# Kernel optimization log

Measured on AMD Instinct MI355X. Metric: run time of the kernel, lower is better.

The kernel has to match this reference:

```python
import jax, jax.numpy as jnp
import numpy as np

NEG_SLOPE = 0.2


def _segment_softmax(logits, seg, num_segments):
    m = jax.ops.segment_max(logits, seg, num_segments=num_segments)
    m = jnp.where(jnp.isfinite(m), m, 0.0)
    e = jnp.exp(logits - m[seg])
    s = jax.ops.segment_sum(e, seg, num_segments=num_segments)
    return e / (s[seg] + 1e-16)


def _gat_conv(x, src, dst, W, a_src, a_dst, b, num_nodes):
    # PyG GATConv, heads=1, concat=True, add_self_loops already applied to src/dst.
    h = x @ W                                  # [N, F_out]
    alpha_src = h @ a_src                      # [N]
    alpha_dst = h @ a_dst                      # [N]
    logits = jax.nn.leaky_relu(alpha_src[src] + alpha_dst[dst], NEG_SLOPE)  # [E]
    alpha = _segment_softmax(logits, dst, num_nodes)                        # [E]
    out = jax.ops.segment_sum(alpha[:, None] * h[src], dst, num_segments=num_nodes)
    return out + b


def setup_inputs() -> dict:
    key = jax.random.key(0)
    ks = jax.random.split(key, 16)
    N, E, F_in = 50000, 1600000, 256
    x = jax.random.normal(ks[0], (N, F_in), dtype=jnp.float32)
    edge_index = jax.random.randint(ks[1], (2, E), 0, N, dtype=jnp.int64)
    edge_attr = jax.random.normal(ks[2], (E, 1), dtype=jnp.float32)

    def glorot(k, shape):
        fan = sum(shape) if len(shape) > 1 else shape[0]
        return jax.random.normal(k, shape, dtype=jnp.float32) * jnp.sqrt(2.0 / fan)

    params = {
        "W1": glorot(ks[3], (F_in, 48)), "as1": glorot(ks[4], (48,)),
        "ad1": glorot(ks[5], (48,)),     "b1": jnp.zeros((48,), jnp.float32),
        "W2": glorot(ks[6], (48, 60)),   "as2": glorot(ks[7], (60,)),
        "ad2": glorot(ks[8], (60,)),     "b2": jnp.zeros((60,), jnp.float32),
        "W3": glorot(ks[9], (60, 1)),    "as3": glorot(ks[10], (1,)),
        "ad3": glorot(ks[11], (1,)),     "b3": jnp.zeros((1,), jnp.float32),
    }
    return {"x": x, "edge_index": edge_index, "edge_attr": edge_attr, **params}


def reference(x, edge_index, edge_attr, W1, as1, ad1, b1, W2, as2, ad2, b2, W3, as3, ad3, b3):
    # edge_attr is accepted but ignored: GATConv was built without edge_dim, so no lin_edge.
    N = x.shape[0]
    loops = jnp.arange(N, dtype=edge_index.dtype)
    src = jnp.concatenate([edge_index[0], loops])  # add_self_loops=True
    dst = jnp.concatenate([edge_index[1], loops])
    h = jax.nn.relu(_gat_conv(x, src, dst, W1, as1, ad1, b1, N))
    h = jax.nn.relu(_gat_conv(h, src, dst, W2, as2, ad2, b2, N))
    h = _gat_conv(h, src, dst, W3, as3, ad3, b3, N)
    return h.reshape(-1)  # flatten -> [N]
```

## Files before the change

kernel.cpp:

```cpp
#include <hip/hip_runtime.h>
#include <cstdint>
#include <cstddef>


__device__ __forceinline__ float leaky(float v) { return v > 0.f ? v : 0.2f * v; }

__device__ __forceinline__ unsigned short f2bf(float x) {
    unsigned int u = __float_as_uint(x);
    u = (u + 0x7FFFu + ((u >> 16) & 1u)) >> 16;
    return (unsigned short)u;
}
__device__ __forceinline__ float bf2f(unsigned short b) {
    return __uint_as_float(((unsigned int)b) << 16);
}

#define BSHIFT 7
#define BCAP   5120
#define CTILE  8192


__global__ __launch_bounds__(256) void coarse_bin_kernel(
    const int* __restrict__ ei, unsigned int* __restrict__ staged,
    int* __restrict__ gcursor, int E, int K) {
    __shared__ int hist[512];
    __shared__ int rank[512];
    __shared__ int base[512];
    for (int b = threadIdx.x; b < K; b += 256) { hist[b] = 0; rank[b] = 0; }
    __syncthreads();

    int e0 = blockIdx.x * CTILE;
    int e1 = min(E, e0 + CTILE);

    for (int e = e0 + threadIdx.x; e < e1; e += 256) {
        int d = ei[E + e];
        atomicAdd(&hist[d >> BSHIFT], 1);
    }
    __syncthreads();

    for (int b = threadIdx.x; b < K; b += 256) {
        int c = hist[b];
        base[b] = c ? atomicAdd(&gcursor[b], c) : 0;
    }
    __syncthreads();

    for (int e = e0 + threadIdx.x; e < e1; e += 256) {
        int s = ei[e];
        int d = ei[E + e];
        int b = d >> BSHIFT;
        int r = atomicAdd(&rank[b], 1);
        staged[(size_t)b * BCAP + base[b] + r] =
            ((unsigned int)(d & ((1 << BSHIFT) - 1)) << 16) | (unsigned int)s;
    }
}


__global__ __launch_bounds__(512) void bucket_scan_kernel(
    const int* __restrict__ gcursor, int* __restrict__ bbase, int K) {
    __shared__ int sh[512];
    int t = threadIdx.x;
    int v = (t < K) ? gcursor[t] : 0;
    sh[t] = v;
    __syncthreads();
    for (int off = 1; off < 512; off <<= 1) {
        int a = (t >= off) ? sh[t - off] : 0;
        __syncthreads();
        sh[t] += a;
        __syncthreads();
    }
    if (t < K) bbase[t] = sh[t] - v;
}


__global__ __launch_bounds__(256) void fine_sort_kernel(
    const unsigned int* __restrict__ staged, const int* __restrict__ gcursor,
    const int* __restrict__ bbase, int* __restrict__ rowptr, int* __restrict__ csr,
    int N, int E) {
    __shared__ int cnt[128];
    __shared__ int off[128];
    __shared__ int lcsr[BCAP];
    const int b = blockIdx.x;
    const int t = threadIdx.x;
    const int c = gcursor[b];
    const int gb = bbase[b];
    const unsigned int* rec = staged + (size_t)b * BCAP;

    if (t < 128) cnt[t] = 0;
    __syncthreads();

    for (int i = t; i < c; i += 256) atomicAdd(&cnt[rec[i] >> 16], 1);
    __syncthreads();

    if (t < 128) off[t] = cnt[t];
    __syncthreads();
    for (int s = 1; s < 128; s <<= 1) {
        int a = (t >= s && t < 128) ? off[t - s] : 0;
        __syncthreads();
        if (t < 128) off[t] += a;
        __syncthreads();
    }

    if (t < 128) {
        int excl = off[t] - cnt[t];
        int n = (b << BSHIFT) + t;
        if (n <= N) rowptr[n] = gb + excl;
        cnt[t] = excl;
    }
    if (b == 0 && t == 0) rowptr[N] = E;
    __syncthreads();

    for (int i = t; i < c; i += 256) {
        unsigned int r = rec[i];
        int p = atomicAdd(&cnt[r >> 16], 1);
        lcsr[p] = (int)(r & 0xFFFFu);
    }
    __syncthreads();

    for (int i = t; i < c; i += 256) csr[gb + i] = lcsr[i];
}


template <int FIN, int FOUT, int FT, int KT>
__global__ __launch_bounds__(256) void gemm_dbuf_kernel(
    const float* __restrict__ X, const float* __restrict__ W,
    const float* __restrict__ avs, const float* __restrict__ avd,
    unsigned short* __restrict__ hb, float* __restrict__ asrc, float* __restrict__ adst,
    int N) {
    static_assert(4 * FT == FOUT, "FT must be FOUT/4");
    static_assert(FIN % KT == 0, "KT must divide FIN");
    constexpr int NC = FIN / KT;
    constexpr int PITCH = KT + 4;
    constexpr int NF4 = KT / 4;
    constexpr int TOT4 = 64 * NF4;
    constexpr int PER_T = TOT4 / 256;
    constexpr int NBUF = (NC > 1) ? 2 : 1;
    __shared__ float xs[NBUF][64][PITCH];
    __shared__ float red[2][4][64];

    const int tid  = threadIdx.x;
    const int wid  = __builtin_amdgcn_readfirstlane(tid >> 6);
    const int lane = tid & 63;
    const int n    = blockIdx.x * 64 + lane;
    const int fbase = wid * FT;

    int snode[PER_T], sk4[PER_T];
    const float* srow[PER_T];
#pragma unroll
    for (int i = 0; i < PER_T; i++) {
        int idx = tid + i * 256;
        snode[i] = idx / NF4;
        sk4[i]   = idx % NF4;
        int nr = blockIdx.x * 64 + snode[i];
        if (nr > N - 1) nr = N - 1;
        srow[i] = X + (size_t)nr * FIN + sk4[i] * 4;
    }

    float acc[FT];
#pragma unroll
    for (int c = 0; c < FT; c++) acc[c] = 0.f;

#pragma unroll
    for (int i = 0; i < PER_T; i++) {
        float4 v = *(const float4*)(srow[i]);
        *(float4*)&xs[0][snode[i]][sk4[i] * 4] = v;
    }
    __syncthreads();

    for (int c0 = 0; c0 < NC; c0++) {
        const int cur = (NBUF == 2) ? (c0 & 1) : 0;
        float4 pf[PER_T];
        if (NBUF == 2 && c0 + 1 < NC) {
#pragma unroll
            for (int i = 0; i < PER_T; i++)
                pf[i] = *(const float4*)(srow[i] + (size_t)(c0 + 1) * KT);
        }

        const int kc = c0 * KT;
#pragma unroll 4
        for (int kk = 0; kk < KT; kk += 4) {
            float4 xv = *(const float4*)&xs[cur][lane][kk];
            const float* w0 = W + (size_t)(kc + kk) * FOUT + fbase;
#pragma unroll
            for (int c = 0; c < FT; c++) {
                acc[c] = fmaf(xv.x, w0[c],            acc[c]);
                acc[c] = fmaf(xv.y, w0[FOUT + c],     acc[c]);
                acc[c] = fmaf(xv.z, w0[2 * FOUT + c], acc[c]);
                acc[c] = fmaf(xv.w, w0[3 * FOUT + c], acc[c]);
            }
        }

        if (NBUF == 2 && c0 + 1 < NC) {
#pragma unroll
            for (int i = 0; i < PER_T; i++)
                *(float4*)&xs[cur ^ 1][snode[i]][sk4[i] * 4] = pf[i];
            __syncthreads();
        }
    }

    float ps = 0.f, pd = 0.f;
#pragma unroll
    for (int c = 0; c < FT; c++) {
        ps = fmaf(acc[c], avs[fbase + c], ps);
        pd = fmaf(acc[c], avd[fbase + c], pd);
    }
    red[0][wid][lane] = ps;
    red[1][wid][lane] = pd;

    if (n < N) {
        if constexpr ((FT & 1) == 0) {
            unsigned int* dst = (unsigned int*)(hb + (size_t)n * 64 + fbase);
#pragma unroll
            for (int c = 0; c < FT; c += 2) {
                unsigned int pk = (unsigned int)f2bf(acc[c]) |
                                  ((unsigned int)f2bf(acc[c + 1]) << 16);
                dst[c >> 1] = pk;
            }
        } else {
#pragma unroll
            for (int c = 0; c < FT; c++)
                hb[(size_t)n * 64 + fbase + c] = f2bf(acc[c]);
        }
    }

    __syncthreads();
    if (tid < 64 && n < N) {
        float s = red[0][0][lane] + red[0][1][lane] + red[0][2][lane] + red[0][3][lane];
        float d = red[1][0][lane] + red[1][1][lane] + red[1][2][lane] + red[1][3][lane];
        asrc[n] = s;
        adst[n] = d;
    }
}


#define CHUNK 128

template <int FOUT, bool RELU>
__global__ __launch_bounds__(256) void agg_bf16_kernel(
    const int* __restrict__ rowptr, const int* __restrict__ csr,
    const float* __restrict__ asrc, const float* __restrict__ adst,
    const unsigned short* __restrict__ hb, const float* __restrict__ bias,
    float* __restrict__ OUT, int N) {
    __shared__ int2 wslds[4][CHUNK];
    const int wv = threadIdx.x >> 6;
    int n = blockIdx.x * 4 + wv;
    if (n >= N) return;
    const int lane = threadIdx.x & 63;
    const int rs = rowptr[n], re = rowptr[n + 1];
    const float ad_n = adst[n];
    const float wself = __expf(leaky(asrc[n] + ad_n));
    const int fc = (lane < FOUT) ? lane : FOUT - 1;

    float acc = wself * bf2f(hb[(size_t)n * 64 + fc]);
    float wpart = 0.f;

    for (int base = rs; base < re; base += CHUNK) {
        const int cnt = min(CHUNK, re - base);
        if (lane < cnt) {
            int s = csr[base + lane];
            float w = __expf(leaky(asrc[s] + ad_n));
            wpart += w;
            wslds[wv][lane] = make_int2(s, __float_as_int(w));
        }
        int i = 0;
        for (; i + 8 <= cnt; i += 8) {
            int2 p[8];
#pragma unroll
            for (int u = 0; u < 8; u++) p[u] = wslds[wv][i + u];
            float hv[8];
#pragma unroll
            for (int u = 0; u < 8; u++) hv[u] = bf2f(hb[(size_t)p[u].x * 64 + fc]);
#pragma unroll
            for (int u = 0; u < 8; u++) acc = fmaf(__int_as_float(p[u].y), hv[u], acc);
        }
        for (; i < cnt; i++) {
            int2 pp = wslds[wv][i];
            acc = fmaf(__int_as_float(pp.y), bf2f(hb[(size_t)pp.x * 64 + fc]), acc);
        }
    }

#pragma unroll
    for (int off = 32; off; off >>= 1) wpart += __shfl_xor(wpart, off, 64);
    float ssum = wpart + wself;

    if (lane < FOUT) {
        float o = acc / (ssum + 1e-16f) + bias[lane];
        if (RELU) o = fmaxf(o, 0.f);
        OUT[(size_t)n * FOUT + lane] = o;
    }
}


__global__ __launch_bounds__(256) void agg_bf16_h3_kernel(
    const int* __restrict__ rowptr, const int* __restrict__ csr,
    const float* __restrict__ asrc, const float* __restrict__ adst,
    const unsigned short* __restrict__ hb, const float* __restrict__ bias,
    const float* __restrict__ W3, float* __restrict__ h3, int N) {
    constexpr int FOUT = 60;
    __shared__ int2 wslds[4][CHUNK];
    const int wv = threadIdx.x >> 6;
    int n = blockIdx.x * 4 + wv;
    if (n >= N) return;
    const int lane = threadIdx.x & 63;
    const int rs = rowptr[n], re = rowptr[n + 1];
    const float ad_n = adst[n];
    const float wself = __expf(leaky(asrc[n] + ad_n));
    const int fc = (lane < FOUT) ? lane : FOUT - 1;

    float acc = wself * bf2f(hb[(size_t)n * 64 + fc]);
    float wpart = 0.f;

    for (int base = rs; base < re; base += CHUNK) {
        const int cnt = min(CHUNK, re - base);
        if (lane < cnt) {
            int s = csr[base + lane];
            float w = __expf(leaky(asrc[s] + ad_n));
            wpart += w;
            wslds[wv][lane] = make_int2(s, __float_as_int(w));
        }
        int i = 0;
        for (; i + 8 <= cnt; i += 8) {
            int2 p[8];
#pragma unroll
            for (int u = 0; u < 8; u++) p[u] = wslds[wv][i + u];
            float hv[8];
#pragma unroll
            for (int u = 0; u < 8; u++) hv[u] = bf2f(hb[(size_t)p[u].x * 64 + fc]);
#pragma unroll
            for (int u = 0; u < 8; u++) acc = fmaf(__int_as_float(p[u].y), hv[u], acc);
        }
        for (; i < cnt; i++) {
            int2 pp = wslds[wv][i];
            acc = fmaf(__int_as_float(pp.y), bf2f(hb[(size_t)pp.x * 64 + fc]), acc);
        }
    }

#pragma unroll
    for (int off = 32; off; off >>= 1) wpart += __shfl_xor(wpart, off, 64);
    float ssum = wpart + wself;

    float t = 0.f;
    if (lane < FOUT) {
        float o = fmaxf(acc / (ssum + 1e-16f) + bias[lane], 0.f);
        t = o * W3[lane];
    }
#pragma unroll
    for (int off = 32; off; off >>= 1) t += __shfl_xor(t, off, 64);
    if (lane == 0) h3[n] = t;
}


__global__ __launch_bounds__(256) void agg1_kernel(
    const int* __restrict__ rowptr, const int* __restrict__ csr,
    const float* __restrict__ h3,
    const float* __restrict__ as3p, const float* __restrict__ ad3p,
    const float* __restrict__ bias, float* __restrict__ OUT, int N) {
    int n = blockIdx.x * 4 + (threadIdx.x >> 6);
    if (n >= N) return;
    int lane = threadIdx.x & 63;
    int rs = rowptr[n], re = rowptr[n + 1];
    const float a_s = as3p[0];
    float hn = h3[n];
    float adn = ad3p[0] * hn;
    float wself = __expf(leaky(a_s * hn + adn));

    float ssum = 0.f, accv = 0.f;
    for (int e = rs + lane; e < re; e += 64) {
        float hs = h3[csr[e]];
        float w = __expf(leaky(a_s * hs + adn));
        ssum += w;
        accv = fmaf(w, hs, accv);
    }
#pragma unroll
    for (int off = 32; off; off >>= 1) {
        ssum += __shfl_xor(ssum, off, 64);
        accv += __shfl_xor(accv, off, 64);
    }
    ssum += wself;
    accv = fmaf(wself, hn, accv);
    if (lane == 0) OUT[n] = accv / (ssum + 1e-16f) + bias[0];
}


extern "C" void kernel_launch(void* const* d_in, const int* in_sizes, int n_in,
                              void* d_out, int out_size, void* d_ws, size_t ws_size,
                              hipStream_t stream) {
    const float* x      = (const float*)d_in[0];
    const int*   ei     = (const int*)d_in[1];
    const float* W1  = (const float*)d_in[3];
    const float* as1 = (const float*)d_in[4];
    const float* ad1 = (const float*)d_in[5];
    const float* b1  = (const float*)d_in[6];
    const float* W2  = (const float*)d_in[7];
    const float* as2 = (const float*)d_in[8];
    const float* ad2 = (const float*)d_in[9];
    const float* b2  = (const float*)d_in[10];
    const float* W3  = (const float*)d_in[11];
    const float* as3 = (const float*)d_in[12];
    const float* ad3 = (const float*)d_in[13];
    const float* b3  = (const float*)d_in[14];

    const int N = in_sizes[0] / 256;
    const int E = in_sizes[1] / 2;
    const int K = (N + (1 << BSHIFT) - 1) >> BSHIFT;

    char* p = (char*)d_ws;
    auto alloc = [&](size_t bytes) -> void* {
        void* r = (void*)p;
        p += ((bytes + 255) / 256) * 256;
        return r;
    };
    int*   gcursor = (int*)alloc(512 * 4);
    int*   bbase   = (int*)alloc(512 * 4);
    int*   rowptr  = (int*)alloc(((size_t)N + 1) * 4);
    int*   csr     = (int*)alloc((size_t)E * 4);
    unsigned short* hb = (unsigned short*)alloc((size_t)N * 64 * 2);
    float* actbuf  = (float*)alloc((size_t)N * 48 * 4);
    float* h3      = (float*)alloc((size_t)N * 4);
    float* asrc    = (float*)alloc((size_t)N * 4);
    float* adst    = (float*)alloc((size_t)N * 4);
    unsigned int* staged = (unsigned int*)actbuf;

    hipMemsetAsync(gcursor, 0, 512 * 4, stream);
    int cblocks = (E + CTILE - 1) / CTILE;
    coarse_bin_kernel<<<cblocks, 256, 0, stream>>>(ei, staged, gcursor, E, K);
    bucket_scan_kernel<<<1, 512, 0, stream>>>(gcursor, bbase, K);
    fine_sort_kernel<<<K, 256, 0, stream>>>(staged, gcursor, bbase, rowptr, csr, N, E);

    int gblocks = (N + 63) / 64;
    int ablocks = (N + 3) / 4;

    gemm_dbuf_kernel<256, 48, 12, 64><<<gblocks, 256, 0, stream>>>(
        x, W1, as1, ad1, hb, asrc, adst, N);
    agg_bf16_kernel<48, true><<<ablocks, 256, 0, stream>>>(rowptr, csr, asrc, adst, hb, b1, actbuf, N);

    gemm_dbuf_kernel<48, 60, 15, 48><<<gblocks, 256, 0, stream>>>(
        actbuf, W2, as2, ad2, hb, asrc, adst, N);
    agg_bf16_h3_kernel<<<ablocks, 256, 0, stream>>>(rowptr, csr, asrc, adst, hb, b2, W3, h3, N);

    agg1_kernel<<<ablocks, 256, 0, stream>>>(rowptr, csr, h3, as3, ad3, b3, (float*)d_out, N);
}
```

Before: 298.8 us.

## Stage GEMM weights in shared memory with double buffering and padded output width

The node-feature GEMM kernel now copies each K-chunk of W into LDS alongside the X tile, double-buffered and prefetched one chunk ahead. The inner loop then reads weights as float4 from LDS instead of as per-element global loads. Layer 2's 60 output columns are zero-padded to 64 so every wave handles 16 columns in float4 groups and packed bf16 stores. The K tile of layer 1 drops from 64 to 32. The trade-off is extra LDS use and copy traffic, which may lower occupancy and could lose to the wave-uniform scalar weight loads the old code relied on.

Measured after the change: 307.7 us. 3.0% more time.

```diff
diff --git a/kernel.cpp b/kernel.cpp
--- a/kernel.cpp
+++ b/kernel.cpp
@@ -119,21 +119,23 @@
 }
 
 
-template <int FIN, int FOUT, int FT, int KT>
-__global__ __launch_bounds__(256) void gemm_dbuf_kernel(
+template <int FIN, int FOUTR, int FOUTP, int FT, int KT>
+__global__ __launch_bounds__(256) void gemm_lw_kernel(
     const float* __restrict__ X, const float* __restrict__ W,
     const float* __restrict__ avs, const float* __restrict__ avd,
     unsigned short* __restrict__ hb, float* __restrict__ asrc, float* __restrict__ adst,
     int N) {
-    static_assert(4 * FT == FOUT, "FT must be FOUT/4");
+    static_assert(4 * FT == FOUTP, "FT must be FOUTP/4");
     static_assert(FIN % KT == 0, "KT must divide FIN");
     constexpr int NC = FIN / KT;
-    constexpr int PITCH = KT + 4;
+    constexpr int XPITCH = KT + 4;
     constexpr int NF4 = KT / 4;
-    constexpr int TOT4 = 64 * NF4;
-    constexpr int PER_T = TOT4 / 256;
+    constexpr int PER_T = (64 * NF4) / 256;
+    constexpr int WTOT4 = (KT * FOUTP) / 4;
+    constexpr int WPT = (WTOT4 + 255) / 256;
     constexpr int NBUF = (NC > 1) ? 2 : 1;
-    __shared__ float xs[NBUF][64][PITCH];
+    __shared__ float xs[NBUF][64][XPITCH];
+    __shared__ float ws[NBUF][KT][FOUTP];
     __shared__ float red[2][4][64];
 
     const int tid  = threadIdx.x;
@@ -163,35 +165,68 @@
         float4 v = *(const float4*)(srow[i]);
         *(float4*)&xs[0][snode[i]][sk4[i] * 4] = v;
     }
-    __syncthreads();
-
+    if constexpr (FOUTR == FOUTP) {
+#pragma unroll
+        for (int i = 0; i < WPT; i++) {
+            int idx = tid + i * 256;
+            if (idx < WTOT4) {
+                float4 v = *(const float4*)(W + (size_t)idx * 4);
+                *(float4*)&(&ws[0][0][0])[idx * 4] = v;
+            }
+        }
+    } else {
+        for (int i = tid; i < KT * FOUTP; i += 256) {
+            int k = i / FOUTP, f = i % FOUTP;
+            (&ws[0][0][0])[i] = (f < FOUTR) ? W[(size_t)k * FOUTR + f] : 0.f;
+        }
+    }
+    __syncthreads();
+
+#pragma unroll 1
     for (int c0 = 0; c0 < NC; c0++) {
         const int cur = (NBUF == 2) ? (c0 & 1) : 0;
-        float4 pf[PER_T];
+        float4 pfx[PER_T];
+        float4 pfw[WPT];
         if (NBUF == 2 && c0 + 1 < NC) {
 #pragma unroll
             for (int i = 0; i < PER_T; i++)
-                pf[i] = *(const float4*)(srow[i] + (size_t)(c0 + 1) * KT);
-        }
-
-        const int kc = c0 * KT;
+                pfx[i] = *(const float4*)(srow[i] + (size_t)(c0 + 1) * KT);
+            const float* wsrc = W + (size_t)(c0 + 1) * KT * FOUTR;
+#pragma unroll
+            for (int i = 0; i < WPT; i++) {
+                int idx = tid + i * 256;
+                if (idx < WTOT4) pfw[i] = *(const float4*)(wsrc + (size_t)idx * 4);
+            }
+        }
+
 #pragma unroll 4
         for (int kk = 0; kk < KT; kk += 4) {
             float4 xv = *(const float4*)&xs[cur][lane][kk];
-            const float* w0 = W + (size_t)(kc + kk) * FOUT + fbase;
-#pragma unroll
-            for (int c = 0; c < FT; c++) {
-                acc[c] = fmaf(xv.x, w0[c],            acc[c]);
-                acc[c] = fmaf(xv.y, w0[FOUT + c],     acc[c]);
-                acc[c] = fmaf(xv.z, w0[2 * FOUT + c], acc[c]);
-                acc[c] = fmaf(xv.w, w0[3 * FOUT + c], acc[c]);
+#pragma unroll
+            for (int r = 0; r < 4; r++) {
+                float xr = (r == 0) ? xv.x : (r == 1) ? xv.y : (r == 2) ? xv.z : xv.w;
+                const float* wrow = &ws[cur][kk + r][fbase];
+#pragma unroll
+                for (int c4 = 0; c4 < FT / 4; c4++) {
+                    float4 wv = *(const float4*)(wrow + c4 * 4);
+                    acc[c4 * 4 + 0] = fmaf(xr, wv.x, acc[c4 * 4 + 0]);
+                    acc[c4 * 4 + 1] = fmaf(xr, wv.y, acc[c4 * 4 + 1]);
+                    acc[c4 * 4 + 2] = fmaf(xr, wv.z, acc[c4 * 4 + 2]);
+                    acc[c4 * 4 + 3] = fmaf(xr, wv.w, acc[c4 * 4 + 3]);
+                }
             }
         }
 
         if (NBUF == 2 && c0 + 1 < NC) {
+            const int nxt = cur ^ 1;
 #pragma unroll
             for (int i = 0; i < PER_T; i++)
-                *(float4*)&xs[cur ^ 1][snode[i]][sk4[i] * 4] = pf[i];
+                *(float4*)&xs[nxt][snode[i]][sk4[i] * 4] = pfx[i];
+#pragma unroll
+            for (int i = 0; i < WPT; i++) {
+                int idx = tid + i * 256;
+                if (idx < WTOT4) *(float4*)&(&ws[nxt][0][0])[idx * 4] = pfw[i];
+            }
             __syncthreads();
         }
     }
@@ -199,25 +234,21 @@
     float ps = 0.f, pd = 0.f;
 #pragma unroll
     for (int c = 0; c < FT; c++) {
-        ps = fmaf(acc[c], avs[fbase + c], ps);
-        pd = fmaf(acc[c], avd[fbase + c], pd);
+        if (FOUTR == FOUTP || fbase + c < FOUTR) {
+            ps = fmaf(acc[c], avs[fbase + c], ps);
+            pd = fmaf(acc[c], avd[fbase + c], pd);
+        }
     }
     red[0][wid][lane] = ps;
     red[1][wid][lane] = pd;
 
     if (n < N) {
-        if constexpr ((FT & 1) == 0) {
-            unsigned int* dst = (unsigned int*)(hb + (size_t)n * 64 + fbase);
-#pragma unroll
-            for (int c = 0; c < FT; c += 2) {
-                unsigned int pk = (unsigned int)f2bf(acc[c]) |
-                                  ((unsigned int)f2bf(acc[c + 1]) << 16);
-                dst[c >> 1] = pk;
-            }
-        } else {
-#pragma unroll
-            for (int c = 0; c < FT; c++)
-                hb[(size_t)n * 64 + fbase + c] = f2bf(acc[c]);
+        unsigned int* dst = (unsigned int*)(hb + (size_t)n * 64 + fbase);
+#pragma unroll
+        for (int c = 0; c < FT; c += 2) {
+            unsigned int pk = (unsigned int)f2bf(acc[c]) |
+                              ((unsigned int)f2bf(acc[c + 1]) << 16);
+            dst[c >> 1] = pk;
         }
     }
 
@@ -428,11 +459,11 @@
     int gblocks = (N + 63) / 64;
     int ablocks = (N + 3) / 4;
 
-    gemm_dbuf_kernel<256, 48, 12, 64><<<gblocks, 256, 0, stream>>>(
+    gemm_lw_kernel<256, 48, 48, 12, 32><<<gblocks, 256, 0, stream>>>(
         x, W1, as1, ad1, hb, asrc, adst, N);
     agg_bf16_kernel<48, true><<<ablocks, 256, 0, stream>>>(rowptr, csr, asrc, adst, hb, b1, actbuf, N);
 
-    gemm_dbuf_kernel<48, 60, 15, 48><<<gblocks, 256, 0, stream>>>(
+    gemm_lw_kernel<48, 60, 64, 16, 48><<<gblocks, 256, 0, stream>>>(
         actbuf, W2, as2, ad2, hb, asrc, adst, N);
     agg_bf16_h3_kernel<<<ablocks, 256, 0, stream>>>(rowptr, csr, asrc, adst, hb, b2, W3, h3, N);
 
```
